# Kernel optimization log

Measured on AMD Instinct MI355X. Metric: run time of the kernel, lower is better.

## Reference

```python
import jax, jax.numpy as jnp
import numpy as np

INPUT_SIZE = 1024
OUTPUT_SIZE = 1024
HEADS = 8
FREQ = 10000.0
NEG_INF = -1e9


def absolute_position(T, d, freq):
    # AP[p, 2i] = sin(p / freq^(2i/d)); AP[p, 2i+1] = cos(...). T assumed even.
    pos = jnp.arange(T, dtype=jnp.float32)[:, None]          # [T, 1]
    i = jnp.arange(T // 2, dtype=jnp.float32)[None, :]       # [1, T//2]
    angle = pos / (freq ** (2.0 * i / d))                    # [T, T//2]
    return jnp.stack([jnp.sin(angle), jnp.cos(angle)], axis=-1).reshape(T, T)


def setup_inputs() -> dict:
    key = jax.random.key(0)
    k_x, k_m, k_q, k_k, k_v, k_o = jax.random.split(key, 6)
    bs, n = 4, 2048
    dh = OUTPUT_SIZE // HEADS
    s_in = 1.0 / np.sqrt(INPUT_SIZE)
    s_out = 1.0 / np.sqrt(OUTPUT_SIZE)
    return {
        "x": jax.random.normal(k_x, (bs, n, INPUT_SIZE), dtype=jnp.float32),
        "mask": jax.random.randint(k_m, (bs, n), 0, 2, dtype=jnp.int32),
        # torch Linear weight layout: [out_features, in_features], stacked per head -> [H, dh, D]
        "Wq": jax.random.uniform(k_q, (HEADS, dh, INPUT_SIZE), jnp.float32, -s_in, s_in),
        "Wk": jax.random.uniform(k_k, (HEADS, dh, INPUT_SIZE), jnp.float32, -s_in, s_in),
        "Wv": jax.random.uniform(k_v, (HEADS, dh, INPUT_SIZE), jnp.float32, -s_in, s_in),
        "Wout": jax.random.uniform(k_o, (INPUT_SIZE, OUTPUT_SIZE), jnp.float32, -s_out, s_out),
    }


def reference(x, mask, Wq, Wk, Wv, Wout):
    bs, n, d = x.shape
    # per-head projections (no bias): [b, h, n, dh]
    Q = jnp.einsum('bnd,hed->bhne', x, Wq)
    K = jnp.einsum('bnd,hed->bhne', x, Wk)
    V = jnp.einsum('bnd,hed->bhne', x, Wv)
    # unscaled scores, as in the original module
    energies = jnp.einsum('bhqe,bhke->bhqk', Q, K)             # [b, h, n, n]
    AP = absolute_position(n, d, FREQ)                         # [n, n]
    energies = energies + AP
    m = mask.astype(bool)
    attn_mask = m[:, None, :, None] & m[:, None, None, :]      # [b, 1, n, n]
    energies = jnp.where(attn_mask, energies, NEG_INF)
    A = jax.nn.softmax(energies, axis=-1)                      # [b, h, n, n]
    # original computes (V^T @ A)^T == A^T @ V  (note transposed attention)
    y = jnp.einsum('bhji,bhje->bhie', A, V)                    # [b, h, n, dh]
    y = y.transpose(0, 2, 1, 3).reshape(bs, n, -1)             # concat heads -> [b, n, D]
    out = jnp.einsum('bnd,od->bno', y, Wout)
    return out, A[:, -1]  # original returns last head's att_weights
```

## Files before the change

### kernel.cpp

```cpp
#include <hip/hip_runtime.h>
#include <math.h>

#define BS_ 4
#define N_  2048
#define D_  1024
#define H_  8
#define DH_ 128

typedef __attribute__((ext_vector_type(8))) short short8;
typedef __attribute__((ext_vector_type(4))) short short4_t;
typedef __attribute__((ext_vector_type(4))) float float4_t;
typedef unsigned short u16;

__device__ __forceinline__ u16 f2bf(float f) {
    union { float f; unsigned u; } v; v.f = f;
    unsigned r = v.u + 0x7FFFu + ((v.u >> 16) & 1u);
    return (u16)(r >> 16);
}
__device__ __forceinline__ float bf2f(u16 h) {
    union { unsigned u; float f; } v; v.u = ((unsigned)h) << 16;
    return v.f;
}
__device__ __forceinline__ void split4(float a, float b, float c, float d,
                                       short4_t* hi, short4_t* lo) {
    u16 h0 = f2bf(a), h1 = f2bf(b), h2 = f2bf(c), h3 = f2bf(d);
    (*hi)[0] = (short)h0; (*hi)[1] = (short)h1; (*hi)[2] = (short)h2; (*hi)[3] = (short)h3;
    (*lo)[0] = (short)f2bf(a - bf2f(h0));
    (*lo)[1] = (short)f2bf(b - bf2f(h1));
    (*lo)[2] = (short)f2bf(c - bf2f(h2));
    (*lo)[3] = (short)f2bf(d - bf2f(h3));
}

__device__ __forceinline__ void gl_lds16(const void* g, void* l) {
    __builtin_amdgcn_global_load_lds(
        (const __attribute__((address_space(1))) unsigned int*)g,
        (__attribute__((address_space(3))) unsigned int*)l,
        16, 0, 0);
}

__global__ void apt_kernel(unsigned int* __restrict__ APtw) {
    int idx = blockIdx.x * 256 + threadIdx.x;
    int i = idx >> 10;
    int jw = idx & 1023;
    int u = i >> 1;
    float ex = exp2f(-(float)u * (13.287712379549449f / 512.0f));
    float a0 = (float)(2 * jw) * ex;
    float a1 = (float)(2 * jw + 1) * ex;
    float v0, v1;
    if (i & 1) { v0 = cosf(a0); v1 = cosf(a1); }
    else       { v0 = sinf(a0); v1 = sinf(a1); }
    APtw[(size_t)i * (N_ / 2) + jw] = (unsigned)f2bf(v0) | ((unsigned)f2bf(v1) << 16);
}

__global__ void split_kernel(const float* __restrict__ x,
                             const float* __restrict__ Wq, const float* __restrict__ Wk,
                             const float* __restrict__ Wv, const float* __restrict__ Wo,
                             u16* __restrict__ Xhi, u16* __restrict__ Xlo,
                             u16* __restrict__ Whi, u16* __restrict__ Wlo,
                             u16* __restrict__ Wvhi, u16* __restrict__ Wohi) {
    int i = blockIdx.x * 256 + threadIdx.x;
    const float* src; u16 *dhi, *dlo; size_t off;
    if (i < 2097152)      { src = x  + 4*(size_t)i;             dhi = Xhi;  dlo = Xlo;  off = 4*(size_t)i; }
    else if (i < 2359296) { size_t j = i - 2097152; src = Wq + 4*j; dhi = Whi; dlo = Wlo; off = 4*j; }
    else if (i < 2621440) { size_t j = i - 2359296; src = Wk + 4*j; dhi = Whi; dlo = Wlo; off = 1048576 + 4*j; }
    else if (i < 2883584) { size_t j = i - 2621440; src = Wv + 4*j; dhi = Wvhi; dlo = nullptr; off = 4*j; }
    else                  { size_t j = i - 2883584; src = Wo + 4*j; dhi = Wohi; dlo = nullptr; off = 4*j; }
    float4 v = *(const float4*)src;
    short4_t hi, lo;
    split4(v.x, v.y, v.z, v.w, &hi, &lo);
    *(short4_t*)(dhi + off) = hi;
    if (dlo) *(short4_t*)(dlo + off) = lo;
}

__global__ __launch_bounds__(256, 4) void qk_gemm(
    const u16* __restrict__ Xhi, const u16* __restrict__ Xlo,
    const u16* __restrict__ Whi, const u16* __restrict__ Wlo,
    u16* __restrict__ Qhi, u16* __restrict__ Qlo,
    u16* __restrict__ Khi, u16* __restrict__ Klo)
{
    const int mt = blockIdx.x;
    const int nt = blockIdx.y;
    const int tid = threadIdx.x, wave = tid >> 6, lane = tid & 63;
    const int quad = lane >> 4, l16 = lane & 15;

    __shared__ __align__(16) u16 sA[2][128 * 32];
    __shared__ __align__(16) u16 sB[2][128 * 32];

    const int srow = lane >> 2;
    const int scol = (lane & 3) * 8;
    const size_t aoff = ((size_t)(mt * 128) + srow) * 1024 + scol;
    const size_t boff = ((size_t)(nt * 128) + srow) * 1024 + scol;
    const int r0 = wave * 16, r1 = 64 + wave * 16;

    float4_t acc[2][8];
#pragma unroll
    for (int i = 0; i < 2; ++i)
#pragma unroll
        for (int j = 0; j < 8; ++j) acc[i][j] = (float4_t)(0.f);

    for (int kt = 0; kt < 32; ++kt) {
        __syncthreads();
        const int kc0 = kt * 32;
        gl_lds16(Xhi + aoff + (size_t)r0 * 1024 + kc0, &sA[0][r0 * 32]);
        gl_lds16(Xhi + aoff + (size_t)r1 * 1024 + kc0, &sA[0][r1 * 32]);
        gl_lds16(Xlo + aoff + (size_t)r0 * 1024 + kc0, &sA[1][r0 * 32]);
        gl_lds16(Xlo + aoff + (size_t)r1 * 1024 + kc0, &sA[1][r1 * 32]);
        gl_lds16(Whi + boff + (size_t)r0 * 1024 + kc0, &sB[0][r0 * 32]);
        gl_lds16(Whi + boff + (size_t)r1 * 1024 + kc0, &sB[0][r1 * 32]);
        gl_lds16(Wlo + boff + (size_t)r0 * 1024 + kc0, &sB[1][r0 * 32]);
        gl_lds16(Wlo + boff + (size_t)r1 * 1024 + kc0, &sB[1][r1 * 32]);
        __syncthreads();

#pragma unroll
        for (int t = 0; t < 3; ++t) {
            const u16* As = sA[t == 2 ? 1 : 0];
            const u16* Bs = sB[t == 1 ? 1 : 0];
            short8 afr[2];
#pragma unroll
            for (int mi = 0; mi < 2; ++mi)
                afr[mi] = *(const short8*)(As + (wave * 32 + mi * 16 + l16) * 32 + quad * 8);
#pragma unroll
            for (int ne = 0; ne < 8; ++ne) {
                short8 bfr = *(const short8*)(Bs + (ne * 16 + l16) * 32 + quad * 8);
#pragma unroll
                for (int mi = 0; mi < 2; ++mi)
                    acc[mi][ne] = __builtin_amdgcn_mfma_f32_16x16x32_bf16(afr[mi], bfr, acc[mi][ne], 0, 0, 0);
            }
        }
    }

    const int b = mt >> 4, q0 = (mt & 15) * 128;
    const bool isQ = (nt < 8);
    u16* Hi = isQ ? Qhi : Khi;
    u16* Lo = isQ ? Qlo : Klo;
    const int h = isQ ? nt : nt - 8;
    const size_t base = (size_t)(b * 8 + h) * N_ * DH_;
#pragma unroll
    for (int mi = 0; mi < 2; ++mi)
#pragma unroll
        for (int ne = 0; ne < 8; ++ne)
#pragma unroll
            for (int r = 0; r < 4; ++r) {
                int q = q0 + wave * 32 + mi * 16 + quad * 4 + r;
                int e = ne * 16 + l16;
                float v = acc[mi][ne][r];
                u16 hv = f2bf(v);
                Hi[base + (size_t)q * DH_ + e] = hv;
                Lo[base + (size_t)q * DH_ + e] = f2bf(v - bf2f(hv));
            }
}

__global__ __launch_bounds__(256, 4) void v_gemm(
    const u16* __restrict__ Wvhi, const u16* __restrict__ Xhi,
    u16* __restrict__ VT)
{
    const int qt = blockIdx.x;
    const int bh = blockIdx.y;
    const int b = bh >> 3, h = bh & 7;
    const int tid = threadIdx.x, wave = tid >> 6, lane = tid & 63;
    const int quad = lane >> 4, l16 = lane & 15;

    __shared__ __align__(16) u16 sA[128 * 32];
    __shared__ __align__(16) u16 sB[128 * 32];

    const int srow = lane >> 2, scol = (lane & 3) * 8;
    const size_t aoff = ((size_t)(h * 128) + srow) * 1024 + scol;
    const size_t boff = ((size_t)(b * N_ + qt * 128) + srow) * 1024 + scol;
    const int r0 = wave * 16, r1 = 64 + wave * 16;

    float4_t acc[2][8];
#pragma unroll
    for (int i = 0; i < 2; ++i)
#pragma unroll
        for (int j = 0; j < 8; ++j) acc[i][j] = (float4_t)(0.f);

    for (int kt = 0; kt < 32; ++kt) {
        __syncthreads();
        const int kc0 = kt * 32;
        gl_lds16(Wvhi + aoff + (size_t)r0 * 1024 + kc0, &sA[r0 * 32]);
        gl_lds16(Wvhi + aoff + (size_t)r1 * 1024 + kc0, &sA[r1 * 32]);
        gl_lds16(Xhi  + boff + (size_t)r0 * 1024 + kc0, &sB[r0 * 32]);
        gl_lds16(Xhi  + boff + (size_t)r1 * 1024 + kc0, &sB[r1 * 32]);
        __syncthreads();

        short8 afr[2];
#pragma unroll
        for (int mi = 0; mi < 2; ++mi)
            afr[mi] = *(const short8*)(sA + (wave * 32 + mi * 16 + l16) * 32 + quad * 8);
#pragma unroll
        for (int ne = 0; ne < 8; ++ne) {
            short8 bfr = *(const short8*)(sB + (ne * 16 + l16) * 32 + quad * 8);
#pragma unroll
            for (int mi = 0; mi < 2; ++mi)
                acc[mi][ne] = __builtin_amdgcn_mfma_f32_16x16x32_bf16(afr[mi], bfr, acc[mi][ne], 0, 0, 0);
        }
    }

    u16* Cg = VT + (size_t)bh * DH_ * N_;
#pragma unroll
    for (int mi = 0; mi < 2; ++mi)
#pragma unroll
        for (int ne = 0; ne < 8; ++ne)
#pragma unroll
            for (int r = 0; r < 4; ++r) {
                int e = wave * 32 + mi * 16 + quad * 4 + r;
                int q = qt * 128 + ne * 16 + l16;
                Cg[(size_t)e * N_ + q] = f2bf(acc[mi][ne][r]);
            }
}

__global__ __launch_bounds__(512, 4) void rowstats_kernel(
    const u16* __restrict__ Qhi, const u16* __restrict__ Qlo,
    const u16* __restrict__ Khi, const u16* __restrict__ Klo,
    const u16* __restrict__ APt,
    const int* __restrict__ mask,
    float* __restrict__ lrow)
{
    const int jt = blockIdx.x;
    const int bh = blockIdx.y;
    const int b = bh >> 3;
    const int tid = threadIdx.x, wave = tid >> 6, lane = tid & 63;
    const int quad = lane >> 4, l16 = lane & 15;
    const int jsub = (wave & 3) * 16, khalf = wave >> 2;

    __shared__ __align__(16) u16 ldsK[2][64 * 264];
    __shared__ int   s_mk[2][64];
    __shared__ float psum[64 * 2];

    short8 rQh[4], rQl[4];
    {
        const size_t qrow = ((size_t)bh * N_ + (size_t)(jt * 64 + jsub + l16)) * DH_;
#pragma unroll
        for (int kc = 0; kc < 4; ++kc) {
            rQh[kc] = *(const short8*)(Qhi + qrow + kc * 32 + quad * 8);
            rQl[kc] = *(const short8*)(Qlo + qrow + kc * 32 + quad * 8);
        }
    }

    const u16* ap_base = APt + (size_t)(khalf * 32 + l16) * N_ + jt * 64 + jsub + quad * 4;
    short4_t apc[2];
#pragma unroll
    for (int nk = 0; nk < 2; ++nk)
        apc[nk] = *(const short4_t*)(ap_base + (size_t)(nk * 16) * N_);

    {
        const size_t Kb = ((size_t)bh * N_) * DH_;
        for (int c = tid; c < 2048; c += 512) {
            int row = c >> 5, half = (c >> 4) & 1, seg = c & 15;
            *(short8*)(ldsK[0] + row * 264 + half * 128 + seg * 8) =
                *(const short8*)((half ? Klo : Khi) + Kb + (size_t)row * DH_ + seg * 8);
        }
        if (tid < 64) s_mk[0][tid] = mask[b * N_ + tid];
    }

    float p[4] = {0.f, 0.f, 0.f, 0.f};
    int mj_on[4];
#pragma unroll
    for (int r = 0; r < 4; ++r)
        mj_on[r] = mask[b * N_ + jt * 64 + jsub + quad * 4 + r];

    __syncthreads();

    for (int kt = 0; kt < 32; ++kt) {
        const int cur = kt & 1, nxt = cur ^ 1;
        short8 rK[4];
        short4_t apn[2];
        int rmk = 0;
        if (kt < 31) {
            const size_t Kb2 = ((size_t)bh * N_ + (size_t)(kt + 1) * 64) * DH_;
#pragma unroll
            for (int i = 0; i < 4; ++i) {
                int c = tid + i * 512;
                int row = c >> 5, half = (c >> 4) & 1, seg = c & 15;
                rK[i] = *(const short8*)((half ? Klo : Khi) + Kb2 + (size_t)row * DH_ + seg * 8);
            }
#pragma unroll
            for (int nk = 0; nk < 2; ++nk)
                apn[nk] = *(const short4_t*)(ap_base + (size_t)((kt + 1) * 64 + nk * 16) * N_);
            if (tid < 64) rmk = mask[b * N_ + (kt + 1) * 64 + tid];
        }

        float4_t accA[2][2];
#pragma unroll
        for (int hf = 0; hf < 2; ++hf) {
            accA[hf][0] = (float4_t)(0.f); accA[hf][1] = (float4_t)(0.f);
        }
        __builtin_amdgcn_s_setprio(1);
#pragma unroll
        for (int kc = 0; kc < 4; ++kc) {
            const int hf = kc >> 1;
            short8 bH[2], bL[2];
#pragma unroll
            for (int nk = 0; nk < 2; ++nk)
                bH[nk] = *(const short8*)(ldsK[cur] + (khalf * 32 + nk * 16 + l16) * 264 + kc * 32 + quad * 8);
#pragma unroll
            for (int nk = 0; nk < 2; ++nk)
                accA[hf][nk] = __builtin_amdgcn_mfma_f32_16x16x32_bf16(rQh[kc], bH[nk], accA[hf][nk], 0, 0, 0);
#pragma unroll
            for (int nk = 0; nk < 2; ++nk)
                accA[hf][nk] = __builtin_amdgcn_mfma_f32_16x16x32_bf16(rQl[kc], bH[nk], accA[hf][nk], 0, 0, 0);
#pragma unroll
            for (int nk = 0; nk < 2; ++nk)
                bL[nk] = *(const short8*)(ldsK[cur] + (khalf * 32 + nk * 16 + l16) * 264 + 128 + kc * 32 + quad * 8);
#pragma unroll
            for (int nk = 0; nk < 2; ++nk)
                accA[hf][nk] = __builtin_amdgcn_mfma_f32_16x16x32_bf16(rQh[kc], bL[nk], accA[hf][nk], 0, 0, 0);
        }
        __builtin_amdgcn_s_setprio(0);
        float4_t acc[2];
        acc[0] = accA[0][0] + accA[1][0];
        acc[1] = accA[0][1] + accA[1][1];

#pragma unroll
        for (int nk = 0; nk < 2; ++nk) {
            int kk = khalf * 32 + nk * 16 + l16;
            int mk = s_mk[cur][kk];
#pragma unroll
            for (int r = 0; r < 4; ++r) {
                float e = acc[nk][r] + bf2f((u16)apc[nk][r]);
                e = (mj_on[r] && mk) ? e : -1.0e9f;
                p[r] += __expf(e);
            }
        }

        if (kt < 31) {
#pragma unroll
            for (int i = 0; i < 4; ++i) {
                int c = tid + i * 512;
                int row = c >> 5, half = (c >> 4) & 1, seg = c & 15;
                *(short8*)(ldsK[nxt] + row * 264 + half * 128 + seg * 8) = rK[i];
            }
            if (tid < 64) s_mk[nxt][tid] = rmk;
            apc[0] = apn[0]; apc[1] = apn[1];
        }
        __syncthreads();
    }

#pragma unroll
    for (int r = 0; r < 4; ++r) {
        float s = p[r];
        for (int off = 1; off < 16; off <<= 1)
            s += __shfl_xor(s, off, 64);
        if (l16 == 0)
            psum[(jsub + quad * 4 + r) * 2 + khalf] = s;
    }
    __syncthreads();
    if (tid < 64)
        lrow[(size_t)bh * N_ + jt * 64 + tid] = psum[tid * 2] + psum[tid * 2 + 1];
}

__global__ __launch_bounds__(512, 2) void attn_kernel(
    const u16* __restrict__ Qhi, const u16* __restrict__ Qlo,
    const u16* __restrict__ Khi, const u16* __restrict__ Klo,
    const u16* __restrict__ VT,
    const u16* __restrict__ APt,
    const int* __restrict__ mask,
    const float* __restrict__ lrow,
    u16* __restrict__ yout,
    float* __restrict__ aout)
{
    const int it = blockIdx.x;
    const int bh = blockIdx.y;
    const int b = bh >> 3, h = bh & 7;
    const int tid = threadIdx.x, wave = tid >> 6, lane = tid & 63;
    const int quad = lane >> 4, l16 = lane & 15;

    __shared__ __align__(16) u16 ldsQ[2][64 * 264];
    __shared__ __align__(16) u16 ldsV[2][128 * 64];
    __shared__ __align__(16) u16 ldsA[128 * 72];
    __shared__ __align__(16) float s_g[2][64];

    const int iq = wave >> 1, jh = wave & 1;
    const int igv0 = it * 128 + iq * 32 + l16;
    const int igv1 = igv0 + 16;
    const size_t vbase = (size_t)bh * DH_ * N_;

    short8 rKh[4][2], rKl[4][2];
    {
        const size_t kr0 = ((size_t)bh * N_ + igv0) * DH_;
        const size_t kr1 = ((size_t)bh * N_ + igv1) * DH_;
#pragma unroll
        for (int kc = 0; kc < 4; ++kc) {
            rKh[kc][0] = *(const short8*)(Khi + kr0 + kc * 32 + quad * 8);
            rKh[kc][1] = *(const short8*)(Khi + kr1 + kc * 32 + quad * 8);
            rKl[kc][0] = *(const short8*)(Klo + kr0 + kc * 32 + quad * 8);
            rKl[kc][1] = *(const short8*)(Klo + kr1 + kc * 32 + quad * 8);
        }
    }

    const u16* apb0 = APt + (size_t)igv0 * N_ + jh * 32 + quad * 4;
    const u16* apb1 = APt + (size_t)igv1 * N_ + jh * 32 + quad * 4;
    short4_t apc[2][2];
#pragma unroll
    for (int mj = 0; mj < 2; ++mj) {
        apc[0][mj] = *(const short4_t*)(apb0 + mj * 16);
        apc[1][mj] = *(const short4_t*)(apb1 + mj * 16);
    }

    const int ion0 = mask[b * N_ + igv0];
    const int ion1 = mask[b * N_ + igv1];

    {
        const size_t Qb0 = ((size_t)bh * N_) * DH_;
        for (int c = tid; c < 2048; c += 512) {
            int row = c >> 5, half = (c >> 4) & 1, seg = c & 15;
            *(short8*)(ldsQ[0] + row * 264 + half * 128 + seg * 8) =
                *(const short8*)((half ? Qlo : Qhi) + Qb0 + (size_t)row * DH_ + seg * 8);
        }
#pragma unroll
        for (int i = 0; i < 2; ++i) {
            int c = i * 512 + wave * 64 + lane;
            int e = c >> 3, g = c & 7;
            gl_lds16(VT + vbase + (size_t)e * N_ + ((g ^ (e & 7)) * 8),
                     ldsV[0] + (size_t)(i * 512 + wave * 64) * 8);
        }
        if (tid < 64) {
            float l = lrow[(size_t)bh * N_ + tid];
            int mj = mask[b * N_ + tid];
            s_g[0][tid] = (mj && l > 0.f) ? 1.0f / l : -1.0f;
        }
    }

    float4_t accy[2][4];
#pragma unroll
    for (int ni = 0; ni < 2; ++ni)
#pragma unroll
        for (int ne = 0; ne < 4; ++ne) accy[ni][ne] = (float4_t)(0.f);

    const bool do_aout = (h == 7);
    const float inv_n = 1.0f / (float)N_;

    __syncthreads();

    for (int jt = 0; jt < 32; ++jt) {
        const int cur = jt & 1, nxt = cur ^ 1;
        const int j0 = jt * 64;

        short8 rQ[4];
        short4_t apn[2][2];
        float r_g = 0.f;
        if (jt < 31) {
            const int j0n = j0 + 64;
#pragma unroll
            for (int i = 0; i < 2; ++i) {
                int c = i * 512 + wave * 64 + lane;
                int e = c >> 3, g = c & 7;
                gl_lds16(VT + vbase + (size_t)e * N_ + j0n + ((g ^ (e & 7)) * 8),
                         ldsV[nxt] + (size_t)(i * 512 + wave * 64) * 8);
            }
            const size_t Qb2 = ((size_t)bh * N_ + j0n) * DH_;
#pragma unroll
            for (int i = 0; i < 4; ++i) {
                int c = tid + i * 512;
                int row = c >> 5, half = (c >> 4) & 1, seg = c & 15;
                rQ[i] = *(const short8*)((half ? Qlo : Qhi) + Qb2 + (size_t)row * DH_ + seg * 8);
            }
#pragma unroll
            for (int mj = 0; mj < 2; ++mj) {
                apn[0][mj] = *(const short4_t*)(apb0 + j0n + mj * 16);
                apn[1][mj] = *(const short4_t*)(apb1 + j0n + mj * 16);
            }
            if (tid < 64) {
                float l = lrow[(size_t)bh * N_ + j0n + tid];
                int mj = mask[b * N_ + j0n + tid];
                r_g = (mj && l > 0.f) ? 1.0f / l : -1.0f;
            }
        }

        float4_t accsA[2][2][2];
#pragma unroll
        for (int hf = 0; hf < 2; ++hf)
#pragma unroll
            for (int mj = 0; mj < 2; ++mj)
#pragma unroll
                for (int ih = 0; ih < 2; ++ih) accsA[hf][mj][ih] = (float4_t)(0.f);

        __builtin_amdgcn_s_setprio(1);
#pragma unroll
        for (int kc = 0; kc < 4; ++kc) {
            const int hf = kc >> 1;
            short8 aH[2], aL[2];
#pragma unroll
            for (int mj = 0; mj < 2; ++mj)
                aH[mj] = *(const short8*)(ldsQ[cur] + (jh * 32 + mj * 16 + l16) * 264 + kc * 32 + quad * 8);
#pragma unroll
            for (int mj = 0; mj < 2; ++mj)
#pragma unroll
                for (int ih = 0; ih < 2; ++ih)
                    accsA[hf][mj][ih] = __builtin_amdgcn_mfma_f32_16x16x32_bf16(aH[mj], rKh[kc][ih], accsA[hf][mj][ih], 0, 0, 0);
#pragma unroll
            for (int mj = 0; mj < 2; ++mj)
                aL[mj] = *(const short8*)(ldsQ[cur] + (jh * 32 + mj * 16 + l16) * 264 + 128 + kc * 32 + quad * 8);
#pragma unroll
            for (int mj = 0; mj < 2; ++mj)
#pragma unroll
                for (int ih = 0; ih < 2; ++ih)
                    accsA[hf][mj][ih] = __builtin_amdgcn_mfma_f32_16x16x32_bf16(aL[mj], rKh[kc][ih], accsA[hf][mj][ih], 0, 0, 0);
#pragma unroll
            for (int mj = 0; mj < 2; ++mj)
#pragma unroll
                for (int ih = 0; ih < 2; ++ih)
                    accsA[hf][mj][ih] = __builtin_amdgcn_mfma_f32_16x16x32_bf16(aH[mj], rKl[kc][ih], accsA[hf][mj][ih], 0, 0, 0);
        }
        __builtin_amdgcn_s_setprio(0);

#pragma unroll
        for (int mj = 0; mj < 2; ++mj) {
            float4_t g4 = *(const float4_t*)(&s_g[cur][jh * 32 + mj * 16 + quad * 4]);
#pragma unroll
            for (int ih = 0; ih < 2; ++ih) {
                float4_t accs = accsA[0][mj][ih] + accsA[1][mj][ih];
                const int ig = ih ? igv1 : igv0;
                const int ion = ih ? ion1 : ion0;
                short4_t pk;
#pragma unroll
                for (int r = 0; r < 4; ++r) {
                    int jl = jh * 32 + mj * 16 + quad * 4 + r;
                    float e = accs[r] + bf2f((u16)apc[ih][mj][r]);
                    float g = g4[r];
                    float a = (g < 0.f) ? inv_n : (ion ? __expf(e) * g : 0.f);
                    pk[r] = (short)f2bf(a);
                    if (do_aout)
                        aout[((size_t)(b * N_ + j0 + jl)) * N_ + ig] = a;
                }
                *(short4_t*)(ldsA + (size_t)(iq * 32 + ih * 16 + l16) * 72 + jh * 32 + mj * 16 + quad * 4) = pk;
            }
        }
        __syncthreads();

        {
            short8 afrA[2][2];
#pragma unroll
            for (int ni = 0; ni < 2; ++ni)
#pragma unroll
                for (int ks = 0; ks < 2; ++ks)
                    afrA[ni][ks] = *(const short8*)(ldsA + (iq * 32 + ni * 16 + l16) * 72 + ks * 32 + quad * 8);
            __builtin_amdgcn_s_setprio(1);
#pragma unroll
            for (int ne = 0; ne < 4; ++ne) {
#pragma unroll
                for (int ks = 0; ks < 2; ++ks) {
                    short8 bfr = *(const short8*)(ldsV[cur] + (size_t)(jh * 64 + ne * 16 + l16) * 64 +
                                                  (((ks * 4 + quad) ^ (l16 & 7)) * 8));
#pragma unroll
                    for (int ni = 0; ni < 2; ++ni)
                        accy[ni][ne] = __builtin_amdgcn_mfma_f32_16x16x32_bf16(afrA[ni][ks], bfr, accy[ni][ne], 0, 0, 0);
                }
            }
            __builtin_amdgcn_s_setprio(0);
        }

        if (jt < 31) {
#pragma unroll
            for (int i = 0; i < 4; ++i) {
                int c = tid + i * 512;
                int row = c >> 5, half = (c >> 4) & 1, seg = c & 15;
                *(short8*)(ldsQ[nxt] + row * 264 + half * 128 + seg * 8) = rQ[i];
            }
            if (tid < 64) s_g[nxt][tid] = r_g;
#pragma unroll
            for (int mj = 0; mj < 2; ++mj) {
                apc[0][mj] = apn[0][mj];
                apc[1][mj] = apn[1][mj];
            }
        }
        __syncthreads();
    }

#pragma unroll
    for (int ni = 0; ni < 2; ++ni)
#pragma unroll
        for (int ne = 0; ne < 4; ++ne)
#pragma unroll
            for (int r = 0; r < 4; ++r) {
                int irow = iq * 32 + ni * 16 + quad * 4 + r;
                int e = jh * 64 + ne * 16 + l16;
                yout[((size_t)b * N_ + it * 128 + irow) * D_ + h * DH_ + e] =
                    f2bf(accy[ni][ne][r]);
            }
}

__global__ __launch_bounds__(256, 4) void outgemm_kernel(
    const u16* __restrict__ A,
    const u16* __restrict__ B,
    float* __restrict__ C)
{
    const int nt = blockIdx.x;
    const int mt = blockIdx.y;
    const int tid = threadIdx.x, wave = tid >> 6, lane = tid & 63;
    const int quad = lane >> 4, l16 = lane & 15;

    __shared__ __align__(16) u16 sA[128 * 32];
    __shared__ __align__(16) u16 sB[128 * 32];

    const int srow = lane >> 2, scol = (lane & 3) * 8;
    const size_t aoff = ((size_t)(mt * 128) + srow) * 1024 + scol;
    const size_t boff = ((size_t)(nt * 128) + srow) * 1024 + scol;
    const int r0 = wave * 16, r1 = 64 + wave * 16;

    float4_t acc[2][8];
#pragma unroll
    for (int i = 0; i < 2; ++i)
#pragma unroll
        for (int j = 0; j < 8; ++j) acc[i][j] = (float4_t)(0.f);

    for (int kt = 0; kt < 32; ++kt) {
        __syncthreads();
        const int kc0 = kt * 32;
        gl_lds16(A + aoff + (size_t)r0 * 1024 + kc0, &sA[r0 * 32]);
        gl_lds16(A + aoff + (size_t)r1 * 1024 + kc0, &sA[r1 * 32]);
        gl_lds16(B + boff + (size_t)r0 * 1024 + kc0, &sB[r0 * 32]);
        gl_lds16(B + boff + (size_t)r1 * 1024 + kc0, &sB[r1 * 32]);
        __syncthreads();

        short8 afr[2];
#pragma unroll
        for (int mi = 0; mi < 2; ++mi)
            afr[mi] = *(const short8*)(sA + (wave * 32 + mi * 16 + l16) * 32 + quad * 8);
#pragma unroll
        for (int ne = 0; ne < 8; ++ne) {
            short8 bfr = *(const short8*)(sB + (ne * 16 + l16) * 32 + quad * 8);
#pragma unroll
            for (int mi = 0; mi < 2; ++mi)
                acc[mi][ne] = __builtin_amdgcn_mfma_f32_16x16x32_bf16(afr[mi], bfr, acc[mi][ne], 0, 0, 0);
        }
    }

#pragma unroll
    for (int mi = 0; mi < 2; ++mi)
#pragma unroll
        for (int ne = 0; ne < 8; ++ne)
#pragma unroll
            for (int r = 0; r < 4; ++r) {
                int row = mt * 128 + wave * 32 + mi * 16 + quad * 4 + r;
                int col = nt * 128 + ne * 16 + l16;
                C[(size_t)row * D_ + col] = acc[mi][ne][r];
            }
}

extern "C" void kernel_launch(void* const* d_in, const int* in_sizes, int n_in,
                              void* d_out, int out_size, void* d_ws, size_t ws_size,
                              hipStream_t stream)
{
    const float* x   = (const float*)d_in[0];
    const int*   msk = (const int*)d_in[1];
    const float* Wq  = (const float*)d_in[2];
    const float* Wk  = (const float*)d_in[3];
    const float* Wv  = (const float*)d_in[4];
    const float* Wo  = (const float*)d_in[5];

    float* out  = (float*)d_out;
    float* aout = out + (size_t)BS_ * N_ * D_;

    u16* Whi  = (u16*)d_out;
    u16* Wlo  = Whi  + (size_t)2048 * 1024;
    u16* Wvhi = Wlo  + (size_t)2048 * 1024;
    u16* Xhi  = Wvhi + (size_t)1024 * 1024;
    u16* Xlo  = Xhi  + (size_t)8192 * 1024;

    char* w = (char*)d_ws;
    u16* APt = (u16*)w;                       w += (size_t)N_ * N_ * 2;
    const size_t szqk = (size_t)BS_ * H_ * N_ * DH_ * 2;
    u16* Qhi = (u16*)w; w += szqk;
    u16* Qlo = (u16*)w; w += szqk;
    u16* Khi = (u16*)w; w += szqk;
    u16* Klo = (u16*)w; w += szqk;
    u16* VT  = (u16*)w; w += szqk;
    float* lrow = (float*)w;                  w += (size_t)BS_ * H_ * N_ * 4;
    u16* Wohi = (u16*)w;                      w += (size_t)D_ * D_ * 2;
    u16* yb   = (u16*)w;                      w += (size_t)BS_ * N_ * D_ * 2;

    apt_kernel<<<8192, 256, 0, stream>>>((unsigned int*)APt);
    split_kernel<<<12288, 256, 0, stream>>>(x, Wq, Wk, Wv, Wo,
                                            Xhi, Xlo, Whi, Wlo, Wvhi, Wohi);
    qk_gemm<<<dim3(64, 16), 256, 0, stream>>>(Xhi, Xlo, Whi, Wlo,
                                              Qhi, Qlo, Khi, Klo);
    v_gemm<<<dim3(16, 32), 256, 0, stream>>>(Wvhi, Xhi, VT);
    rowstats_kernel<<<dim3(32, 32), 512, 0, stream>>>(Qhi, Qlo, Khi, Klo, APt, msk, lrow);
    attn_kernel<<<dim3(16, 32), 512, 0, stream>>>(Qhi, Qlo, Khi, Klo, VT, APt, msk,
                                                  lrow, yb, aout);
    outgemm_kernel<<<dim3(8, 64), 256, 0, stream>>>(yb, Wohi, out);
}
```

Before: 638.0 us.

## Software-pipeline attention tiles: defer AV MFMA one step, direct-to-LDS Q loads

Restructures the attention main loop so the A·V product for the previous tile runs before the current tile's softmax epilogue. This removes one __syncthreads per iteration, using a double-buffered A tile and a triple-buffered V tile in LDS. Q loads now go straight from global memory to LDS through swizzled gl_lds16 instead of staging in registers, which frees VGPRs and drops the separate LDS write. A tail block finishes the last AV step. The cost is more LDS use, which may limit occupancy at 2 blocks/CU, plus trickier buffer indexing.

Result: faster. 619.1 us (-3.0%).

```diff
diff --git a/kernel.cpp b/kernel.cpp
--- a/kernel.cpp
+++ b/kernel.cpp
@@ -365,15 +365,17 @@
     const int tid = threadIdx.x, wave = tid >> 6, lane = tid & 63;
     const int quad = lane >> 4, l16 = lane & 15;
 
-    __shared__ __align__(16) u16 ldsQ[2][64 * 264];
-    __shared__ __align__(16) u16 ldsV[2][128 * 64];
-    __shared__ __align__(16) u16 ldsA[128 * 72];
+    __shared__ __align__(16) u16 ldsQ[2 * 64 * 256];
+    __shared__ __align__(16) u16 ldsV[3 * 128 * 64];
+    __shared__ __align__(16) u16 ldsA[2 * 128 * 72];
     __shared__ __align__(16) float s_g[2][64];
 
     const int iq = wave >> 1, jh = wave & 1;
     const int igv0 = it * 128 + iq * 32 + l16;
     const int igv1 = igv0 + 16;
     const size_t vbase = (size_t)bh * DH_ * N_;
+    const size_t qbb = (size_t)bh * N_;
+    const int qsw = l16 & 7;
 
     short8 rKh[4][2], rKl[4][2];
     {
@@ -400,19 +402,24 @@
     const int ion0 = mask[b * N_ + igv0];
     const int ion1 = mask[b * N_ + igv1];
 
+    const int q_rl_off = lane >> 5;
+    const int q_u = lane & 31;
+
     {
-        const size_t Qb0 = ((size_t)bh * N_) * DH_;
-        for (int c = tid; c < 2048; c += 512) {
-            int row = c >> 5, half = (c >> 4) & 1, seg = c & 15;
-            *(short8*)(ldsQ[0] + row * 264 + half * 128 + seg * 8) =
-                *(const short8*)((half ? Qlo : Qhi) + Qb0 + (size_t)row * DH_ + seg * 8);
+#pragma unroll
+        for (int i = 0; i < 4; ++i) {
+            int ch = wave * 4 + i;
+            int rl = 2 * ch + q_rl_off;
+            int u0 = q_u ^ (rl & 7);
+            const u16* src = ((u0 >> 4) ? Qlo : Qhi) + (qbb + rl) * DH_ + (u0 & 15) * 8;
+            gl_lds16(src, ldsQ + ch * 512);
         }
 #pragma unroll
         for (int i = 0; i < 2; ++i) {
             int c = i * 512 + wave * 64 + lane;
             int e = c >> 3, g = c & 7;
             gl_lds16(VT + vbase + (size_t)e * N_ + ((g ^ (e & 7)) * 8),
-                     ldsV[0] + (size_t)(i * 512 + wave * 64) * 8);
+                     ldsV + (size_t)(i * 512 + wave * 64) * 8);
         }
         if (tid < 64) {
             float l = lrow[(size_t)bh * N_ + tid];
@@ -436,24 +443,25 @@
         const int cur = jt & 1, nxt = cur ^ 1;
         const int j0 = jt * 64;
 
-        short8 rQ[4];
         short4_t apn[2][2];
         float r_g = 0.f;
         if (jt < 31) {
             const int j0n = j0 + 64;
+            const int s_wr = (jt + 1) % 3;
 #pragma unroll
             for (int i = 0; i < 2; ++i) {
                 int c = i * 512 + wave * 64 + lane;
                 int e = c >> 3, g = c & 7;
                 gl_lds16(VT + vbase + (size_t)e * N_ + j0n + ((g ^ (e & 7)) * 8),
-                         ldsV[nxt] + (size_t)(i * 512 + wave * 64) * 8);
-            }
-            const size_t Qb2 = ((size_t)bh * N_ + j0n) * DH_;
+                         ldsV + (size_t)s_wr * 8192 + (size_t)(i * 512 + wave * 64) * 8);
+            }
 #pragma unroll
             for (int i = 0; i < 4; ++i) {
-                int c = tid + i * 512;
-                int row = c >> 5, half = (c >> 4) & 1, seg = c & 15;
-                rQ[i] = *(const short8*)((half ? Qlo : Qhi) + Qb2 + (size_t)row * DH_ + seg * 8);
+                int ch = wave * 4 + i;
+                int rl = 2 * ch + q_rl_off;
+                int u0 = q_u ^ (rl & 7);
+                const u16* src = ((u0 >> 4) ? Qlo : Qhi) + (qbb + j0n + rl) * DH_ + (u0 & 15) * 8;
+                gl_lds16(src, ldsQ + nxt * 16384 + ch * 512);
             }
 #pragma unroll
             for (int mj = 0; mj < 2; ++mj) {
@@ -475,6 +483,7 @@
 #pragma unroll
                 for (int ih = 0; ih < 2; ++ih) accsA[hf][mj][ih] = (float4_t)(0.f);
 
+        const u16* qbuf = ldsQ + cur * 16384;
         __builtin_amdgcn_s_setprio(1);
 #pragma unroll
         for (int kc = 0; kc < 4; ++kc) {
@@ -482,7 +491,8 @@
             short8 aH[2], aL[2];
 #pragma unroll
             for (int mj = 0; mj < 2; ++mj)
-                aH[mj] = *(const short8*)(ldsQ[cur] + (jh * 32 + mj * 16 + l16) * 264 + kc * 32 + quad * 8);
+                aH[mj] = *(const short8*)(qbuf + (jh * 32 + mj * 16 + l16) * 256 +
+                                          ((kc * 4 + quad) ^ qsw) * 8);
 #pragma unroll
             for (int mj = 0; mj < 2; ++mj)
 #pragma unroll
@@ -490,7 +500,8 @@
                     accsA[hf][mj][ih] = __builtin_amdgcn_mfma_f32_16x16x32_bf16(aH[mj], rKh[kc][ih], accsA[hf][mj][ih], 0, 0, 0);
 #pragma unroll
             for (int mj = 0; mj < 2; ++mj)
-                aL[mj] = *(const short8*)(ldsQ[cur] + (jh * 32 + mj * 16 + l16) * 264 + 128 + kc * 32 + quad * 8);
+                aL[mj] = *(const short8*)(qbuf + (jh * 32 + mj * 16 + l16) * 256 +
+                                          (((16 + kc * 4 + quad)) ^ qsw) * 8);
 #pragma unroll
             for (int mj = 0; mj < 2; ++mj)
 #pragma unroll
@@ -504,43 +515,21 @@
         }
         __builtin_amdgcn_s_setprio(0);
 
-#pragma unroll
-        for (int mj = 0; mj < 2; ++mj) {
-            float4_t g4 = *(const float4_t*)(&s_g[cur][jh * 32 + mj * 16 + quad * 4]);
-#pragma unroll
-            for (int ih = 0; ih < 2; ++ih) {
-                float4_t accs = accsA[0][mj][ih] + accsA[1][mj][ih];
-                const int ig = ih ? igv1 : igv0;
-                const int ion = ih ? ion1 : ion0;
-                short4_t pk;
-#pragma unroll
-                for (int r = 0; r < 4; ++r) {
-                    int jl = jh * 32 + mj * 16 + quad * 4 + r;
-                    float e = accs[r] + bf2f((u16)apc[ih][mj][r]);
-                    float g = g4[r];
-                    float a = (g < 0.f) ? inv_n : (ion ? __expf(e) * g : 0.f);
-                    pk[r] = (short)f2bf(a);
-                    if (do_aout)
-                        aout[((size_t)(b * N_ + j0 + jl)) * N_ + ig] = a;
-                }
-                *(short4_t*)(ldsA + (size_t)(iq * 32 + ih * 16 + l16) * 72 + jh * 32 + mj * 16 + quad * 4) = pk;
-            }
-        }
-        __syncthreads();
-
-        {
+        if (jt > 0) {
+            const u16* aBuf = ldsA + nxt * 9216;
+            const u16* vBuf = ldsV + ((jt + 2) % 3) * 8192;
             short8 afrA[2][2];
 #pragma unroll
             for (int ni = 0; ni < 2; ++ni)
 #pragma unroll
                 for (int ks = 0; ks < 2; ++ks)
-                    afrA[ni][ks] = *(const short8*)(ldsA + (iq * 32 + ni * 16 + l16) * 72 + ks * 32 + quad * 8);
+                    afrA[ni][ks] = *(const short8*)(aBuf + (iq * 32 + ni * 16 + l16) * 72 + ks * 32 + quad * 8);
             __builtin_amdgcn_s_setprio(1);
 #pragma unroll
             for (int ne = 0; ne < 4; ++ne) {
 #pragma unroll
                 for (int ks = 0; ks < 2; ++ks) {
-                    short8 bfr = *(const short8*)(ldsV[cur] + (size_t)(jh * 64 + ne * 16 + l16) * 64 +
+                    short8 bfr = *(const short8*)(vBuf + (size_t)(jh * 64 + ne * 16 + l16) * 64 +
                                                   (((ks * 4 + quad) ^ (l16 & 7)) * 8));
 #pragma unroll
                     for (int ni = 0; ni < 2; ++ni)
@@ -550,13 +539,33 @@
             __builtin_amdgcn_s_setprio(0);
         }
 
+        {
+            u16* aBufW = ldsA + cur * 9216;
+#pragma unroll
+            for (int mj = 0; mj < 2; ++mj) {
+                float4_t g4 = *(const float4_t*)(&s_g[cur][jh * 32 + mj * 16 + quad * 4]);
+#pragma unroll
+                for (int ih = 0; ih < 2; ++ih) {
+                    float4_t accs = accsA[0][mj][ih] + accsA[1][mj][ih];
+                    const int ig = ih ? igv1 : igv0;
+                    const int ion = ih ? ion1 : ion0;
+                    short4_t pk;
+#pragma unroll
+                    for (int r = 0; r < 4; ++r) {
+                        int jl = jh * 32 + mj * 16 + quad * 4 + r;
+                        float e = accs[r] + bf2f((u16)apc[ih][mj][r]);
+                        float g = g4[r];
+                        float a = (g < 0.f) ? inv_n : (ion ? __expf(e) * g : 0.f);
+                        pk[r] = (short)f2bf(a);
+                        if (do_aout)
+                            aout[((size_t)(b * N_ + j0 + jl)) * N_ + ig] = a;
+                    }
+                    *(short4_t*)(aBufW + (size_t)(iq * 32 + ih * 16 + l16) * 72 + jh * 32 + mj * 16 + quad * 4) = pk;
+                }
+            }
+        }
+
         if (jt < 31) {
-#pragma unroll
-            for (int i = 0; i < 4; ++i) {
-                int c = tid + i * 512;
-                int row = c >> 5, half = (c >> 4) & 1, seg = c & 15;
-                *(short8*)(ldsQ[nxt] + row * 264 + half * 128 + seg * 8) = rQ[i];
-            }
             if (tid < 64) s_g[nxt][tid] = r_g;
 #pragma unroll
             for (int mj = 0; mj < 2; ++mj) {
@@ -565,6 +574,28 @@
             }
         }
         __syncthreads();
+    }
+
+    {
+        const u16* aBuf = ldsA + 1 * 9216;
+        const u16* vBuf = ldsV + 1 * 8192;
+        short8 afrA[2][2];
+#pragma unroll
+        for (int ni = 0; ni < 2; ++ni)
+#pragma unroll
+            for (int ks = 0; ks < 2; ++ks)
+                afrA[ni][ks] = *(const short8*)(aBuf + (iq * 32 + ni * 16 + l16) * 72 + ks * 32 + quad * 8);
+#pragma unroll
+        for (int ne = 0; ne < 4; ++ne) {
+#pragma unroll
+            for (int ks = 0; ks < 2; ++ks) {
+                short8 bfr = *(const short8*)(vBuf + (size_t)(jh * 64 + ne * 16 + l16) * 64 +
+                                              (((ks * 4 + quad) ^ (l16 & 7)) * 8));
+#pragma unroll
+                for (int ni = 0; ni < 2; ++ni)
+                    accy[ni][ne] = __builtin_amdgcn_mfma_f32_16x16x32_bf16(afrA[ni][ks], bfr, accy[ni][ne], 0, 0, 0);
+            }
+        }
     }
 
 #pragma unroll
```
